# Performance work log

Measured on AMD Instinct MI355X. Metric: run time of the kernel, lower is better.

Reference implementation:

```python
import jax, jax.numpy as jnp
import numpy as np

ROPE_BASE = 10000.0
NEG_INF = -1e30


def _rope(x, pos):
    # x: [B, Hx, D], pos: [B] int32. Rotate-half RoPE (non-interleaved).
    D = x.shape[-1]
    inv_freq = 1.0 / (ROPE_BASE ** (jnp.arange(0, D, 2, dtype=jnp.float32) / D))  # [D/2]
    ang = pos.astype(jnp.float32)[:, None] * inv_freq[None, :]                    # [B, D/2]
    emb = jnp.concatenate([ang, ang], axis=-1)                                    # [B, D]
    cos = jnp.cos(emb)[:, None, :]
    sin = jnp.sin(emb)[:, None, :]
    x1, x2 = x[..., : D // 2], x[..., D // 2 :]
    rotated = jnp.concatenate([-x2, x1], axis=-1)
    return x * cos + rotated * sin


def setup_inputs() -> dict:
    key = jax.random.key(0)
    ks = jax.random.split(key, 7)
    B, H, KVH, D = 32, 32, 8, 128
    BLOCK_SIZE, MAX_BLOCKS = 16, 128
    NUM_BLOCKS = B * MAX_BLOCKS  # 4096, disjoint blocks per sequence
    MAX_CTX = BLOCK_SIZE * MAX_BLOCKS  # 2048
    query = jax.random.normal(ks[0], (B, H, D), dtype=jnp.float32)
    new_k = jax.random.normal(ks[1], (B, KVH, D), dtype=jnp.float32)
    new_v = jax.random.normal(ks[2], (B, KVH, D), dtype=jnp.float32)
    k_cache = jax.random.normal(ks[3], (NUM_BLOCKS, BLOCK_SIZE, KVH, D), dtype=jnp.float32)
    v_cache = jax.random.normal(ks[4], (NUM_BLOCKS, BLOCK_SIZE, KVH, D), dtype=jnp.float32)
    block_table = jnp.arange(B * MAX_BLOCKS, dtype=jnp.int32).reshape(B, MAX_BLOCKS)
    context_lens = jnp.clip(jax.random.randint(ks[5], (B,), 0, MAX_CTX, dtype=jnp.int32), 1, MAX_CTX)
    return {"query": query, "key": new_k, "value": new_v,
            "k_cache": k_cache, "v_cache": v_cache,
            "block_table": block_table, "context_lens": context_lens}


def reference(query, key, value, k_cache, v_cache, block_table, context_lens):
    B, H, D = query.shape
    KVH = key.shape[1]
    G = H // KVH  # GQA group size
    block_size = k_cache.shape[1]
    max_blocks = block_table.shape[1]
    S = max_blocks * block_size
    scale = D ** -0.5

    # RoPE at position = context_lens (as in the original module)
    q_rot = _rope(query, context_lens)  # [B, H, D]
    k_rot = _rope(key, context_lens)    # [B, KVH, D]

    # Store new KV at token index context_lens - 1 via block table (paged scatter)
    tok = context_lens - 1
    blk = jnp.take_along_axis(block_table, (tok // block_size)[:, None], axis=1)[:, 0]  # [B]
    off = tok % block_size
    k_cache = k_cache.at[blk, off].set(k_rot)
    v_cache = v_cache.at[blk, off].set(value)

    # Gather per-sequence pages: [B, max_blocks, block_size, KVH, D] -> [B, S, KVH, D]
    K = k_cache[block_table].reshape(B, S, KVH, D)
    V = v_cache[block_table].reshape(B, S, KVH, D)

    # Single-query attention over valid context (positions < context_lens)
    qg = q_rot.reshape(B, KVH, G, D)
    scores = jnp.einsum("bkgd,bskd->bkgs", qg, K) * scale  # [B, KVH, G, S]
    valid = jnp.arange(S, dtype=jnp.int32)[None, :] < context_lens[:, None]  # [B, S]
    scores = jnp.where(valid[:, None, None, :], scores, NEG_INF)
    probs = jax.nn.softmax(scores, axis=-1)
    out = jnp.einsum("bkgs,bskd->bkgd", probs, V).reshape(B, H, D)
    return out
```

## Files before the change

### kernel.cpp

```cpp
#include <hip/hip_runtime.h>
#include <math.h>

#define BATCH 32
#define NH 32
#define NKVH 8
#define GRP 4
#define HD 128
#define BLKSZ 16
#define MAXB 128
#define PART 256
#define NPART 8
#define SCALE 0.08838834764831845f
#define NEGINF (-1e30f)

#define WS_QROT 0
#define WS_KROT (BATCH*NH*HD)
#define WS_ML   (WS_KROT + BATCH*NKVH*HD)
#define WS_OP   (WS_ML + BATCH*NKVH*GRP*NPART*2)

__global__ void rope_prep(const float* __restrict__ q,
                          const float* __restrict__ nk,
                          const int* __restrict__ ctx,
                          float* __restrict__ ws) {
    int b = blockIdx.x;
    int t = threadIdx.x;
    __shared__ float cs[64], sn[64];
    if (t < 64) {
        double f = pow(10000.0, -(double)t / 64.0);
        double a = (double)ctx[b] * f;
        cs[t] = (float)cos(a);
        sn[t] = (float)sin(a);
    }
    __syncthreads();
    int d = t;
    float c = cs[d & 63], s = sn[d & 63];
    for (int h = 0; h < NH; ++h) {
        const float* qp = q + ((size_t)b * NH + h) * HD;
        float x = qp[d];
        float y = qp[d ^ 64];
        float r = (d < 64) ? (x * c - y * s) : (x * c + y * s);
        ws[WS_QROT + ((size_t)b * NH + h) * HD + d] = r;
    }
    for (int kh = 0; kh < NKVH; ++kh) {
        const float* kp = nk + ((size_t)b * NKVH + kh) * HD;
        float x = kp[d];
        float y = kp[d ^ 64];
        float r = (d < 64) ? (x * c - y * s) : (x * c + y * s);
        ws[WS_KROT + ((size_t)b * NKVH + kh) * HD + d] = r;
    }
}

__global__ __launch_bounds__(256)
void attn_partial(const float* __restrict__ kc,
                  const float* __restrict__ vc,
                  const float* __restrict__ nv,
                  const int* __restrict__ btab,
                  const int* __restrict__ ctx,
                  float* __restrict__ ws) {
    int part = blockIdx.x, kvh = blockIdx.y, b = blockIdx.z;
    int L = ctx[b];
    int start = part * PART;
    if (start >= L) return;
    int end = min(start + PART, L);
    int n = end - start;
    int tok = L - 1;

    int tid = threadIdx.x;
    int hw = tid >> 5;
    int hl = tid & 31;
    int wave = tid >> 6;
    int lane = tid & 63;

    __shared__ float sc[GRP][PART];
    __shared__ float oacc[8][GRP][HD];

    const float* qrot = ws + WS_QROT + ((size_t)b * NH + kvh * GRP) * HD;
    float4 qa[GRP];
#pragma unroll
    for (int g = 0; g < GRP; ++g)
        qa[g] = *(const float4*)(qrot + g * HD + 4 * hl);

    const float* krot = ws + WS_KROT + ((size_t)b * NKVH + kvh) * HD;
    const int* bt = btab + b * MAXB;

    for (int s = start + hw; s < end; s += 8) {
        float4 k4;
        if (s == tok) {
            k4 = *(const float4*)(krot + 4 * hl);
        } else {
            int blk = bt[s >> 4];
            const float* kp = kc + (((size_t)blk * BLKSZ + (s & 15)) * NKVH + kvh) * HD;
            k4 = *(const float4*)(kp + 4 * hl);
        }
        float p[GRP];
#pragma unroll
        for (int g = 0; g < GRP; ++g)
            p[g] = qa[g].x * k4.x + qa[g].y * k4.y + qa[g].z * k4.z + qa[g].w * k4.w;
#pragma unroll
        for (int off = 16; off >= 1; off >>= 1) {
#pragma unroll
            for (int g = 0; g < GRP; ++g)
                p[g] += __shfl_xor(p[g], off, 32);
        }
        if (hl == 0) {
#pragma unroll
            for (int g = 0; g < GRP; ++g)
                sc[g][s - start] = p[g] * SCALE;
        }
    }
    __syncthreads();

    {
        int g = wave;
        float m = NEGINF;
        for (int i = lane; i < n; i += 64) m = fmaxf(m, sc[g][i]);
#pragma unroll
        for (int off = 32; off >= 1; off >>= 1) m = fmaxf(m, __shfl_xor(m, off));
        float sum = 0.f;
        for (int i = lane; i < n; i += 64) {
            float e = __expf(sc[g][i] - m);
            sc[g][i] = e;
            sum += e;
        }
#pragma unroll
        for (int off = 32; off >= 1; off >>= 1) sum += __shfl_xor(sum, off);
        if (lane == 0) {
            size_t mlidx = ((((size_t)b * NKVH + kvh) * GRP + g) * NPART + part) * 2;
            ws[WS_ML + mlidx] = m;
            ws[WS_ML + mlidx + 1] = sum;
        }
    }
    __syncthreads();

    float4 acc[GRP];
#pragma unroll
    for (int g = 0; g < GRP; ++g) acc[g] = make_float4(0.f, 0.f, 0.f, 0.f);

    for (int s = start + hw; s < end; s += 8) {
        float4 v4;
        if (s == tok) {
            v4 = *(const float4*)(nv + ((size_t)b * NKVH + kvh) * HD + 4 * hl);
        } else {
            int blk = bt[s >> 4];
            const float* vp = vc + (((size_t)blk * BLKSZ + (s & 15)) * NKVH + kvh) * HD;
            v4 = *(const float4*)(vp + 4 * hl);
        }
        int i = s - start;
#pragma unroll
        for (int g = 0; g < GRP; ++g) {
            float e = sc[g][i];
            acc[g].x += e * v4.x; acc[g].y += e * v4.y;
            acc[g].z += e * v4.z; acc[g].w += e * v4.w;
        }
    }
#pragma unroll
    for (int g = 0; g < GRP; ++g)
        *(float4*)&oacc[hw][g][4 * hl] = acc[g];
    __syncthreads();

    for (int o = tid; o < GRP * HD; o += 256) {
        int g = o >> 7, d = o & 127;
        float ssum = 0.f;
#pragma unroll
        for (int w = 0; w < 8; ++w) ssum += oacc[w][g][d];
        ws[WS_OP + ((((size_t)b * NKVH + kvh) * GRP + g) * NPART + part) * HD + d] = ssum;
    }
}

__global__ __launch_bounds__(128)
void attn_reduce(const int* __restrict__ ctx,
                 const float* __restrict__ ws,
                 float* __restrict__ out) {
    int bh = blockIdx.x;
    int b = bh >> 5;
    int h = bh & 31;
    int kvh = h >> 2, g = h & 3;
    int L = ctx[b];
    int np = min(NPART, (L + PART - 1) / PART);
    size_t base = (((size_t)b * NKVH + kvh) * GRP + g) * NPART;
    float M = NEGINF;
    for (int p = 0; p < np; ++p)
        M = fmaxf(M, ws[WS_ML + (base + p) * 2]);
    float w_[NPART];
    float Lsum = 0.f;
    for (int p = 0; p < np; ++p) {
        float e = __expf(ws[WS_ML + (base + p) * 2] - M);
        w_[p] = e;
        Lsum += e * ws[WS_ML + (base + p) * 2 + 1];
    }
    float inv = 1.0f / Lsum;
    int d = threadIdx.x;
    float acc = 0.f;
    for (int p = 0; p < np; ++p)
        acc += w_[p] * ws[WS_OP + (base + p) * HD + d];
    out[((size_t)b * NH + h) * HD + d] = acc * inv;
}

extern "C" void kernel_launch(void* const* d_in, const int* in_sizes, int n_in,
                              void* d_out, int out_size, void* d_ws, size_t ws_size,
                              hipStream_t stream) {
    const float* q    = (const float*)d_in[0];
    const float* nk   = (const float*)d_in[1];
    const float* nv   = (const float*)d_in[2];
    const float* kc   = (const float*)d_in[3];
    const float* vc   = (const float*)d_in[4];
    const int*   btab = (const int*)d_in[5];
    const int*   ctx  = (const int*)d_in[6];
    float* out = (float*)d_out;
    float* ws  = (float*)d_ws;

    rope_prep<<<dim3(BATCH), dim3(128), 0, stream>>>(q, nk, ctx, ws);
    attn_partial<<<dim3(NPART, NKVH, BATCH), dim3(256), 0, stream>>>(kc, vc, nv, btab, ctx, ws);
    attn_reduce<<<dim3(BATCH * NH), dim3(128), 0, stream>>>(ctx, ws, out);
}
```

Baseline: 510.9 us.

## Fuse RoPE into attention partial kernel and unroll token loops by two

```diff
diff --git a/kernel.cpp b/kernel.cpp
--- a/kernel.cpp
+++ b/kernel.cpp
@@ -13,50 +13,19 @@
 #define SCALE 0.08838834764831845f
 #define NEGINF (-1e30f)
 
-#define WS_QROT 0
-#define WS_KROT (BATCH*NH*HD)
-#define WS_ML   (WS_KROT + BATCH*NKVH*HD)
-#define WS_OP   (WS_ML + BATCH*NKVH*GRP*NPART*2)
-
-__global__ void rope_prep(const float* __restrict__ q,
-                          const float* __restrict__ nk,
-                          const int* __restrict__ ctx,
-                          float* __restrict__ ws) {
-    int b = blockIdx.x;
-    int t = threadIdx.x;
-    __shared__ float cs[64], sn[64];
-    if (t < 64) {
-        double f = pow(10000.0, -(double)t / 64.0);
-        double a = (double)ctx[b] * f;
-        cs[t] = (float)cos(a);
-        sn[t] = (float)sin(a);
-    }
-    __syncthreads();
-    int d = t;
-    float c = cs[d & 63], s = sn[d & 63];
-    for (int h = 0; h < NH; ++h) {
-        const float* qp = q + ((size_t)b * NH + h) * HD;
-        float x = qp[d];
-        float y = qp[d ^ 64];
-        float r = (d < 64) ? (x * c - y * s) : (x * c + y * s);
-        ws[WS_QROT + ((size_t)b * NH + h) * HD + d] = r;
-    }
-    for (int kh = 0; kh < NKVH; ++kh) {
-        const float* kp = nk + ((size_t)b * NKVH + kh) * HD;
-        float x = kp[d];
-        float y = kp[d ^ 64];
-        float r = (d < 64) ? (x * c - y * s) : (x * c + y * s);
-        ws[WS_KROT + ((size_t)b * NKVH + kh) * HD + d] = r;
-    }
-}
+#define WS_ML 0
+#define WS_OP (BATCH*NKVH*GRP*NPART*2)
 
 __global__ __launch_bounds__(256)
-void attn_partial(const float* __restrict__ kc,
-                  const float* __restrict__ vc,
-                  const float* __restrict__ nv,
-                  const int* __restrict__ btab,
-                  const int* __restrict__ ctx,
-                  float* __restrict__ ws) {
+void attn_fused(const float* __restrict__ q,
+                const float* __restrict__ nk,
+                const float* __restrict__ nv,
+                const float* __restrict__ kc,
+                const float* __restrict__ vc,
+                const int* __restrict__ btab,
+                const int* __restrict__ ctx,
+                float* __restrict__ ws)
+{
     int part = blockIdx.x, kvh = blockIdx.y, b = blockIdx.z;
     int L = ctx[b];
     int start = part * PART;
@@ -68,44 +37,85 @@
     int tid = threadIdx.x;
     int hw = tid >> 5;
     int hl = tid & 31;
-    int wave = tid >> 6;
-    int lane = tid & 63;
-
+    int wave = tid >> 6, lane = tid & 63;
+
+    __shared__ float cs[64], sn[64];
+    __shared__ float qs[GRP][HD];
+    __shared__ float ks[HD];
     __shared__ float sc[GRP][PART];
     __shared__ float oacc[8][GRP][HD];
 
-    const float* qrot = ws + WS_QROT + ((size_t)b * NH + kvh * GRP) * HD;
+    if (tid < 64) {
+        double f = pow(10000.0, -(double)tid / 64.0);
+        double a = (double)L * f;
+        cs[tid] = (float)cos(a);
+        sn[tid] = (float)sin(a);
+    }
+    __syncthreads();
+
+    {
+        int g = tid >> 6, d = tid & 63;
+        const float* qp = q + ((size_t)b * NH + kvh * GRP + g) * HD;
+        float x = qp[d], y = qp[d + 64];
+        float c = cs[d], s = sn[d];
+        qs[g][d]      = x * c - y * s;
+        qs[g][d + 64] = y * c + x * s;
+    }
+    if (tok >= start && tok < end && tid < 64) {
+        int d = tid;
+        const float* kp = nk + ((size_t)b * NKVH + kvh) * HD;
+        float x = kp[d], y = kp[d + 64];
+        float c = cs[d], s = sn[d];
+        ks[d]      = x * c - y * s;
+        ks[d + 64] = y * c + x * s;
+    }
+    __syncthreads();
+
     float4 qa[GRP];
 #pragma unroll
     for (int g = 0; g < GRP; ++g)
-        qa[g] = *(const float4*)(qrot + g * HD + 4 * hl);
-
-    const float* krot = ws + WS_KROT + ((size_t)b * NKVH + kvh) * HD;
+        qa[g] = *(const float4*)(&qs[g][4 * hl]);
+
     const int* bt = btab + b * MAXB;
 
-    for (int s = start + hw; s < end; s += 8) {
-        float4 k4;
+    for (int s = start + hw; s < end; s += 16) {
+        int s1 = s + 8;
+        bool h1 = (s1 < end);
+        float4 k0, k1 = make_float4(0.f, 0.f, 0.f, 0.f);
         if (s == tok) {
-            k4 = *(const float4*)(krot + 4 * hl);
+            k0 = *(const float4*)(&ks[4 * hl]);
         } else {
             int blk = bt[s >> 4];
-            const float* kp = kc + (((size_t)blk * BLKSZ + (s & 15)) * NKVH + kvh) * HD;
-            k4 = *(const float4*)(kp + 4 * hl);
-        }
-        float p[GRP];
-#pragma unroll
-        for (int g = 0; g < GRP; ++g)
-            p[g] = qa[g].x * k4.x + qa[g].y * k4.y + qa[g].z * k4.z + qa[g].w * k4.w;
+            k0 = *(const float4*)(kc + (((size_t)blk * BLKSZ + (s & 15)) * NKVH + kvh) * HD + 4 * hl);
+        }
+        if (h1) {
+            if (s1 == tok) {
+                k1 = *(const float4*)(&ks[4 * hl]);
+            } else {
+                int blk = bt[s1 >> 4];
+                k1 = *(const float4*)(kc + (((size_t)blk * BLKSZ + (s1 & 15)) * NKVH + kvh) * HD + 4 * hl);
+            }
+        }
+        float p0[GRP], p1[GRP];
+#pragma unroll
+        for (int g = 0; g < GRP; ++g) {
+            p0[g] = qa[g].x * k0.x + qa[g].y * k0.y + qa[g].z * k0.z + qa[g].w * k0.w;
+            p1[g] = qa[g].x * k1.x + qa[g].y * k1.y + qa[g].z * k1.z + qa[g].w * k1.w;
+        }
 #pragma unroll
         for (int off = 16; off >= 1; off >>= 1) {
 #pragma unroll
-            for (int g = 0; g < GRP; ++g)
-                p[g] += __shfl_xor(p[g], off, 32);
+            for (int g = 0; g < GRP; ++g) {
+                p0[g] += __shfl_xor(p0[g], off, 32);
+                p1[g] += __shfl_xor(p1[g], off, 32);
+            }
         }
         if (hl == 0) {
 #pragma unroll
-            for (int g = 0; g < GRP; ++g)
-                sc[g][s - start] = p[g] * SCALE;
+            for (int g = 0; g < GRP; ++g) {
+                sc[g][s - start] = p0[g] * SCALE;
+                if (h1) sc[g][s1 - start] = p1[g] * SCALE;
+            }
         }
     }
     __syncthreads();
@@ -126,7 +136,7 @@
         for (int off = 32; off >= 1; off >>= 1) sum += __shfl_xor(sum, off);
         if (lane == 0) {
             size_t mlidx = ((((size_t)b * NKVH + kvh) * GRP + g) * NPART + part) * 2;
-            ws[WS_ML + mlidx] = m;
+            ws[WS_ML + mlidx]     = m;
             ws[WS_ML + mlidx + 1] = sum;
         }
     }
@@ -136,21 +146,38 @@
 #pragma unroll
     for (int g = 0; g < GRP; ++g) acc[g] = make_float4(0.f, 0.f, 0.f, 0.f);
 
-    for (int s = start + hw; s < end; s += 8) {
-        float4 v4;
+    for (int s = start + hw; s < end; s += 16) {
+        int s1 = s + 8;
+        bool h1 = (s1 < end);
+        float4 v0, v1 = make_float4(0.f, 0.f, 0.f, 0.f);
         if (s == tok) {
-            v4 = *(const float4*)(nv + ((size_t)b * NKVH + kvh) * HD + 4 * hl);
+            v0 = *(const float4*)(nv + ((size_t)b * NKVH + kvh) * HD + 4 * hl);
         } else {
             int blk = bt[s >> 4];
-            const float* vp = vc + (((size_t)blk * BLKSZ + (s & 15)) * NKVH + kvh) * HD;
-            v4 = *(const float4*)(vp + 4 * hl);
-        }
-        int i = s - start;
+            v0 = *(const float4*)(vc + (((size_t)blk * BLKSZ + (s & 15)) * NKVH + kvh) * HD + 4 * hl);
+        }
+        if (h1) {
+            if (s1 == tok) {
+                v1 = *(const float4*)(nv + ((size_t)b * NKVH + kvh) * HD + 4 * hl);
+            } else {
+                int blk = bt[s1 >> 4];
+                v1 = *(const float4*)(vc + (((size_t)blk * BLKSZ + (s1 & 15)) * NKVH + kvh) * HD + 4 * hl);
+            }
+        }
+        int i0 = s - start, i1 = s1 - start;
 #pragma unroll
         for (int g = 0; g < GRP; ++g) {
-            float e = sc[g][i];
-            acc[g].x += e * v4.x; acc[g].y += e * v4.y;
-            acc[g].z += e * v4.z; acc[g].w += e * v4.w;
+            float e0 = sc[g][i0];
+            acc[g].x += e0 * v0.x; acc[g].y += e0 * v0.y;
+            acc[g].z += e0 * v0.z; acc[g].w += e0 * v0.w;
+        }
+        if (h1) {
+#pragma unroll
+            for (int g = 0; g < GRP; ++g) {
+                float e1 = sc[g][i1];
+                acc[g].x += e1 * v1.x; acc[g].y += e1 * v1.y;
+                acc[g].z += e1 * v1.z; acc[g].w += e1 * v1.w;
+            }
         }
     }
 #pragma unroll
@@ -209,7 +236,6 @@
     float* out = (float*)d_out;
     float* ws  = (float*)d_ws;
 
-    rope_prep<<<dim3(BATCH), dim3(128), 0, stream>>>(q, nk, ctx, ws);
-    attn_partial<<<dim3(NPART, NKVH, BATCH), dim3(256), 0, stream>>>(kc, vc, nv, btab, ctx, ws);
+    attn_fused<<<dim3(NPART, NKVH, BATCH), dim3(256), 0, stream>>>(q, nk, nv, kc, vc, btab, ctx, ws);
     attn_reduce<<<dim3(BATCH * NH), dim3(128), 0, stream>>>(ctx, ws, out);
 }
```

After: 541.1 us. +5.9%, slower.
